# Kernel tuning notes

Measured on AMD Instinct MI355X. Metric: run time of the kernel, lower is better.

## Reference

```python
import jax, jax.numpy as jnp
import numpy as np

S, B, C = 7, 2, 20
LAMBDA_COORD = 5.0
LAMBDA_NOOBJ = 0.5
EPS = 1e-6


def _to_abs_xyxy(boxes):
    # boxes: [..., S, S, 4] cell-relative (x,y,w,h) -> normalized image (x1,y1,x2,y2)
    col = jnp.arange(S, dtype=boxes.dtype)            # broadcasts over last grid axis
    row = jnp.arange(S, dtype=boxes.dtype)[:, None]   # broadcasts over second-to-last grid axis
    x, y, w, h = boxes[..., 0], boxes[..., 1], boxes[..., 2], boxes[..., 3]
    cx = (col + x) / S
    cy = (row + y) / S
    return jnp.stack([cx - w / 2, cy - h / 2, cx + w / 2, cy + h / 2], axis=-1)


def _iou(a, b):
    # elementwise IoU of corresponding xyxy boxes (broadcasting allowed)
    x1 = jnp.maximum(a[..., 0], b[..., 0])
    y1 = jnp.maximum(a[..., 1], b[..., 1])
    x2 = jnp.minimum(a[..., 2], b[..., 2])
    y2 = jnp.minimum(a[..., 3], b[..., 3])
    inter = jnp.clip(x2 - x1, 0.0) * jnp.clip(y2 - y1, 0.0)
    area_a = (a[..., 2] - a[..., 0]) * (a[..., 3] - a[..., 1])
    area_b = (b[..., 2] - b[..., 0]) * (b[..., 3] - b[..., 1])
    return inter / (area_a + area_b - inter + EPS)


def setup_inputs() -> dict:
    key = jax.random.key(0)
    kp, kb, kf, kc = jax.random.split(key, 4)
    bs = 16384
    predictions = jax.random.uniform(kp, (bs, S, S, B * 5 + C), dtype=jnp.float32)
    gt_box = jax.random.uniform(kb, (bs, S, S, 4), dtype=jnp.float32)
    obj = (jax.random.uniform(kf, (bs, S, S)) < 0.06).astype(jnp.float32)
    cls = jax.nn.one_hot(jax.random.randint(kc, (bs, S, S), 0, C), C, dtype=jnp.float32)
    targets = jnp.concatenate([gt_box, obj[..., None], cls], axis=-1)
    return {"predictions": predictions, "targets": targets}


def reference(predictions, targets):
    bs = predictions.shape[0]
    pb = predictions[..., : B * 5].reshape(bs, S, S, B, 5)
    boxes = pb[..., :4]                 # [bs,S,S,B,4]
    confs = pb[..., 4]                  # [bs,S,S,B]
    logits = predictions[..., B * 5 :]  # [bs,S,S,C]

    gt_boxes = targets[..., :4]
    objf = (targets[..., 4] > 0).astype(predictions.dtype)  # [bs,S,S]
    gt_cls = targets[..., 5:]

    # IoU per candidate box vs the cell's GT box
    gt_abs = _to_abs_xyxy(gt_boxes)                         # [bs,S,S,4]
    pred_abs = _to_abs_xyxy(jnp.moveaxis(boxes, 3, 1))      # [bs,B,S,S,4]
    ious = jnp.moveaxis(_iou(pred_abs, gt_abs[:, None]), 1, 3)  # [bs,S,S,B]

    best = jnp.argmax(ious, axis=-1)                        # [bs,S,S]
    resp_box = jnp.take_along_axis(boxes, best[..., None, None], axis=3)[..., 0, :]  # [bs,S,S,4]
    resp_conf = jnp.take_along_axis(confs, best[..., None], axis=-1)[..., 0]
    resp_iou = jnp.take_along_axis(ious, best[..., None], axis=-1)[..., 0]

    # Localization loss (masked-sum == torch boolean-mask + sum reduction)
    w = objf[..., None]
    xy_loss = jnp.sum(w * (resp_box[..., :2] - gt_boxes[..., :2]) ** 2)
    wh_loss = jnp.sum(w * (jnp.sqrt(resp_box[..., 2:4] + EPS) - jnp.sqrt(gt_boxes[..., 2:4] + EPS)) ** 2)
    loss_coord = xy_loss + wh_loss

    # Objectness confidence: target is (detached) IoU of responsible box
    loss_conf_obj = jnp.sum(objf * (resp_conf - jax.lax.stop_gradient(resp_iou)) ** 2)

    # No-object confidence: every (cell, box) that is not the responsible box of an object cell
    resp_mask = jax.nn.one_hot(best, B, dtype=predictions.dtype) * objf[..., None]  # [bs,S,S,B]
    loss_conf_noobj = jnp.sum((1.0 - resp_mask) * confs ** 2)

    # Classification: cross-entropy with one-hot GT, summed over object cells
    logp = jax.nn.log_softmax(logits, axis=-1)
    loss_class = -jnp.sum(objf * jnp.sum(gt_cls * logp, axis=-1))

    n = jnp.asarray(bs, predictions.dtype)
    loss_total = (LAMBDA_COORD * loss_coord + loss_conf_obj + LAMBDA_NOOBJ * loss_conf_noobj + loss_class) / n
    # [loss_coord, loss_conf_obj, loss_conf_noobj, loss_class, loss_total]
    return jnp.stack([loss_coord / n, loss_conf_obj / n, loss_conf_noobj / n, loss_class / n, loss_total])
```

## Files before the change

kernel.cpp:

```cpp
#include <hip/hip_runtime.h>
#include <math.h>

namespace {
constexpr int S = 7;
constexpr int PF = 30;
constexpr int TF = 25;
constexpr int C = 20;
constexpr float EPS = 1e-6f;
constexpr float LAMBDA_COORD = 5.0f;
constexpr float LAMBDA_NOOBJ = 0.5f;
constexpr int BLK = 256;
constexpr int CPT = 4;
}

__global__ __launch_bounds__(BLK) void k_main(const float* __restrict__ pred,
                                              const float* __restrict__ tgt,
                                              float* __restrict__ part,
                                              int n_cells) {
    const int tid = threadIdx.x;
    const int base = blockIdx.x * (BLK * CPT) + tid;

    float2 a45[CPT], a89[CPT];
    float t4[CPT];
    bool ok[CPT];
    #pragma unroll
    for (int k = 0; k < CPT; ++k) {
        const int cell = base + k * BLK;
        ok[k] = (cell < n_cells);
        const float* p = pred + (size_t)cell * PF;
        const float* t = tgt + (size_t)cell * TF;
        if (ok[k]) {
            a45[k] = *(const float2*)(p + 4);
            a89[k] = *(const float2*)(p + 8);
            t4[k]  = t[4];
        } else {
            a45[k] = make_float2(0.f, 0.f);
            a89[k] = make_float2(0.f, 0.f);
            t4[k]  = 0.f;
        }
    }

    float v0 = 0.f, v1 = 0.f, v2 = 0.f, v3 = 0.f;
    #pragma unroll
    for (int k = 0; k < CPT; ++k) {
        const float c0 = a45[k].x, c1 = a89[k].y;
        v2 += c0 * c0 + c1 * c1;

        if (t4[k] > 0.f) {
            const int cell = base + k * BLK;
            const float* p = pred + (size_t)cell * PF;
            const float* t = tgt + (size_t)cell * TF;
            const int j = cell % S;
            const int i = (cell / S) % S;
            const float invS = 1.0f / (float)S;

            const float2 p01 = *(const float2*)(p + 0);
            const float2 p23 = *(const float2*)(p + 2);
            const float2 p67 = *(const float2*)(p + 6);
            const float gx = t[0], gy = t[1], gw = t[2], gh = t[3];

            const float gcx = ((float)j + gx) * invS;
            const float gcy = ((float)i + gy) * invS;
            const float gx1 = gcx - gw * 0.5f, gy1 = gcy - gh * 0.5f;
            const float gx2 = gcx + gw * 0.5f, gy2 = gcy + gh * 0.5f;
            const float garea = (gx2 - gx1) * (gy2 - gy1);

            const float bx[2]  = {p01.x, a45[k].y};
            const float by[2]  = {p01.y, p67.x};
            const float bw_[2] = {p23.x, p67.y};
            const float bh[2]  = {p23.y, a89[k].x};
            const float cf[2]  = {c0, c1};
            float iou[2];
            #pragma unroll
            for (int b = 0; b < 2; ++b) {
                const float cx = ((float)j + bx[b]) * invS;
                const float cy = ((float)i + by[b]) * invS;
                const float x1 = cx - bw_[b] * 0.5f, y1 = cy - bh[b] * 0.5f;
                const float x2 = cx + bw_[b] * 0.5f, y2 = cy + bh[b] * 0.5f;
                const float ix1 = fmaxf(x1, gx1), iy1 = fmaxf(y1, gy1);
                const float ix2 = fminf(x2, gx2), iy2 = fminf(y2, gy2);
                const float inter = fmaxf(ix2 - ix1, 0.f) * fmaxf(iy2 - iy1, 0.f);
                const float parea = (x2 - x1) * (y2 - y1);
                iou[b] = inter / (parea + garea - inter + EPS);
            }
            const int best = (iou[1] > iou[0]) ? 1 : 0;
            const float rconf = cf[best], riou = iou[best];

            const float dx = bx[best] - gx, dy = by[best] - gy;
            const float swd = sqrtf(bw_[best] + EPS) - sqrtf(gw + EPS);
            const float shd = sqrtf(bh[best] + EPS) - sqrtf(gh + EPS);
            v0 += dx * dx + dy * dy + swd * swd + shd * shd;
            const float dc = rconf - riou;
            v1 += dc * dc;
            v2 -= rconf * rconf;

            float se = 0.f, dot = 0.f, sg = 0.f;
            #pragma unroll
            for (int c = 0; c < C; c += 2) {
                const float2 lc = *(const float2*)(p + 10 + c);
                const float g0 = t[5 + c], g1 = t[6 + c];
                se  += __expf(lc.x) + __expf(lc.y);
                dot += g0 * lc.x + g1 * lc.y;
                sg  += g0 + g1;
            }
            v3 += __logf(se) * sg - dot;
        }
    }

    float v[4] = {v0, v1, v2, v3};
    #pragma unroll
    for (int off = 32; off >= 1; off >>= 1) {
        v[0] += __shfl_down(v[0], off, 64);
        v[1] += __shfl_down(v[1], off, 64);
        v[2] += __shfl_down(v[2], off, 64);
        v[3] += __shfl_down(v[3], off, 64);
    }
    __shared__ float red[16];
    if ((tid & 63) == 0) {
        const int wv = tid >> 6;
        red[wv * 4 + 0] = v[0];
        red[wv * 4 + 1] = v[1];
        red[wv * 4 + 2] = v[2];
        red[wv * 4 + 3] = v[3];
    }
    __syncthreads();
    if (tid < 4)
        part[blockIdx.x * 4 + tid] =
            red[tid] + red[4 + tid] + red[8 + tid] + red[12 + tid];
}

__global__ __launch_bounds__(BLK) void k_fin(const float* __restrict__ part,
                                             float* __restrict__ out,
                                             int nblk, float n) {
    const int tid = threadIdx.x;
    float a0 = 0.f, a1 = 0.f, a2 = 0.f, a3 = 0.f;
    for (int r = tid; r < nblk; r += BLK) {
        const float4 q = *(const float4*)(part + r * 4);
        a0 += q.x; a1 += q.y; a2 += q.z; a3 += q.w;
    }
    float v[4] = {a0, a1, a2, a3};
    #pragma unroll
    for (int off = 32; off >= 1; off >>= 1) {
        v[0] += __shfl_down(v[0], off, 64);
        v[1] += __shfl_down(v[1], off, 64);
        v[2] += __shfl_down(v[2], off, 64);
        v[3] += __shfl_down(v[3], off, 64);
    }
    __shared__ float red[16];
    if ((tid & 63) == 0) {
        const int wv = tid >> 6;
        red[wv * 4 + 0] = v[0];
        red[wv * 4 + 1] = v[1];
        red[wv * 4 + 2] = v[2];
        red[wv * 4 + 3] = v[3];
    }
    __syncthreads();
    if (tid == 0) {
        const float coord  = red[0] + red[4] + red[8] + red[12];
        const float cobj   = red[1] + red[5] + red[9] + red[13];
        const float cnoobj = red[2] + red[6] + red[10] + red[14];
        const float ccls   = red[3] + red[7] + red[11] + red[15];
        const float inv = 1.0f / n;
        out[0] = coord * inv;
        out[1] = cobj * inv;
        out[2] = cnoobj * inv;
        out[3] = ccls * inv;
        out[4] = (LAMBDA_COORD * coord + cobj + LAMBDA_NOOBJ * cnoobj + ccls) * inv;
    }
}

extern "C" void kernel_launch(void* const* d_in, const int* in_sizes, int n_in,
                              void* d_out, int out_size, void* d_ws, size_t ws_size,
                              hipStream_t stream) {
    const float* pred = (const float*)d_in[0];
    const float* tgt  = (const float*)d_in[1];
    float* out  = (float*)d_out;
    float* part = (float*)d_ws;

    const int n_cells = in_sizes[0] / PF;
    const float bs = (float)(n_cells / (S * S));
    const int nblk = (n_cells + BLK * CPT - 1) / (BLK * CPT);

    k_main<<<nblk, BLK, 0, stream>>>(pred, tgt, part, n_cells);
    k_fin<<<1, BLK, 0, stream>>>(part, out, nblk, bs);
}
```

Measured before the change: 213.5 us.

## Stage prediction tile through LDS with coalesced float4 loads, one cell per thread

Each block now copies its whole contiguous prediction tile (256 cells x 30 floats) into shared memory with coalesced float4 loads, then each thread reads its cell's fields from LDS. This replaces the earlier scheme of strided float2 loads with four cells per thread. The goal is to turn scattered, latency-bound global accesses into streaming ones. The cost is about 30KB of LDS per block, which limits occupancy, plus an extra barrier, and it loads the full prediction row even for no-object cells.

```diff
diff --git a/kernel.cpp b/kernel.cpp
--- a/kernel.cpp
+++ b/kernel.cpp
@@ -10,65 +10,54 @@
 constexpr float LAMBDA_COORD = 5.0f;
 constexpr float LAMBDA_NOOBJ = 0.5f;
 constexpr int BLK = 256;
-constexpr int CPT = 4;
+constexpr int TILE_F4 = BLK * PF / 4;
 }
 
-__global__ __launch_bounds__(BLK) void k_main(const float* __restrict__ pred,
+__global__ __launch_bounds__(BLK) void k_main(const float4* __restrict__ pred4,
                                               const float* __restrict__ tgt,
                                               float* __restrict__ part,
                                               int n_cells) {
+    __shared__ float sp[BLK * PF];
     const int tid = threadIdx.x;
-    const int base = blockIdx.x * (BLK * CPT) + tid;
+    const int cell = blockIdx.x * BLK + tid;
+    const bool ok = cell < n_cells;
 
-    float2 a45[CPT], a89[CPT];
-    float t4[CPT];
-    bool ok[CPT];
-    #pragma unroll
-    for (int k = 0; k < CPT; ++k) {
-        const int cell = base + k * BLK;
-        ok[k] = (cell < n_cells);
-        const float* p = pred + (size_t)cell * PF;
-        const float* t = tgt + (size_t)cell * TF;
-        if (ok[k]) {
-            a45[k] = *(const float2*)(p + 4);
-            a89[k] = *(const float2*)(p + 8);
-            t4[k]  = t[4];
-        } else {
-            a45[k] = make_float2(0.f, 0.f);
-            a89[k] = make_float2(0.f, 0.f);
-            t4[k]  = 0.f;
+    const float t4 = ok ? tgt[(size_t)cell * TF + 4] : 0.f;
+
+    {
+        const size_t base4 = (size_t)blockIdx.x * TILE_F4;
+        float4* s4 = (float4*)sp;
+        #pragma unroll
+        for (int k = 0; k < 8; ++k) {
+            const int idx = tid + k * BLK;
+            if (idx < TILE_F4) s4[idx] = pred4[base4 + idx];
         }
     }
+    __syncthreads();
 
     float v0 = 0.f, v1 = 0.f, v2 = 0.f, v3 = 0.f;
-    #pragma unroll
-    for (int k = 0; k < CPT; ++k) {
-        const float c0 = a45[k].x, c1 = a89[k].y;
-        v2 += c0 * c0 + c1 * c1;
+    if (ok) {
+        const float* p = sp + tid * PF;
+        const float c0 = p[4], c1 = p[9];
+        v2 = c0 * c0 + c1 * c1;
 
-        if (t4[k] > 0.f) {
-            const int cell = base + k * BLK;
-            const float* p = pred + (size_t)cell * PF;
+        if (t4 > 0.f) {
             const float* t = tgt + (size_t)cell * TF;
             const int j = cell % S;
             const int i = (cell / S) % S;
             const float invS = 1.0f / (float)S;
 
-            const float2 p01 = *(const float2*)(p + 0);
-            const float2 p23 = *(const float2*)(p + 2);
-            const float2 p67 = *(const float2*)(p + 6);
             const float gx = t[0], gy = t[1], gw = t[2], gh = t[3];
-
             const float gcx = ((float)j + gx) * invS;
             const float gcy = ((float)i + gy) * invS;
             const float gx1 = gcx - gw * 0.5f, gy1 = gcy - gh * 0.5f;
             const float gx2 = gcx + gw * 0.5f, gy2 = gcy + gh * 0.5f;
             const float garea = (gx2 - gx1) * (gy2 - gy1);
 
-            const float bx[2]  = {p01.x, a45[k].y};
-            const float by[2]  = {p01.y, p67.x};
-            const float bw_[2] = {p23.x, p67.y};
-            const float bh[2]  = {p23.y, a89[k].x};
+            const float bx[2]  = {p[0], p[5]};
+            const float by[2]  = {p[1], p[6]};
+            const float bw_[2] = {p[2], p[7]};
+            const float bh[2]  = {p[3], p[8]};
             const float cf[2]  = {c0, c1};
             float iou[2];
             #pragma unroll
@@ -89,21 +78,21 @@
             const float dx = bx[best] - gx, dy = by[best] - gy;
             const float swd = sqrtf(bw_[best] + EPS) - sqrtf(gw + EPS);
             const float shd = sqrtf(bh[best] + EPS) - sqrtf(gh + EPS);
-            v0 += dx * dx + dy * dy + swd * swd + shd * shd;
+            v0 = dx * dx + dy * dy + swd * swd + shd * shd;
             const float dc = rconf - riou;
-            v1 += dc * dc;
+            v1 = dc * dc;
             v2 -= rconf * rconf;
 
             float se = 0.f, dot = 0.f, sg = 0.f;
             #pragma unroll
             for (int c = 0; c < C; c += 2) {
-                const float2 lc = *(const float2*)(p + 10 + c);
-                const float g0 = t[5 + c], g1 = t[6 + c];
-                se  += __expf(lc.x) + __expf(lc.y);
-                dot += g0 * lc.x + g1 * lc.y;
+                const float l0 = p[10 + c], l1 = p[11 + c];
+                const float g0 = t[5 + c],  g1 = t[6 + c];
+                se  += __expf(l0) + __expf(l1);
+                dot += g0 * l0 + g1 * l1;
                 sg  += g0 + g1;
             }
-            v3 += __logf(se) * sg - dot;
+            v3 = __logf(se) * sg - dot;
         }
     }
 
@@ -115,18 +104,18 @@
         v[2] += __shfl_down(v[2], off, 64);
         v[3] += __shfl_down(v[3], off, 64);
     }
-    __shared__ float red[16];
+    __syncthreads();
     if ((tid & 63) == 0) {
         const int wv = tid >> 6;
-        red[wv * 4 + 0] = v[0];
-        red[wv * 4 + 1] = v[1];
-        red[wv * 4 + 2] = v[2];
-        red[wv * 4 + 3] = v[3];
+        sp[wv * 4 + 0] = v[0];
+        sp[wv * 4 + 1] = v[1];
+        sp[wv * 4 + 2] = v[2];
+        sp[wv * 4 + 3] = v[3];
     }
     __syncthreads();
     if (tid < 4)
         part[blockIdx.x * 4 + tid] =
-            red[tid] + red[4 + tid] + red[8 + tid] + red[12 + tid];
+            sp[tid] + sp[4 + tid] + sp[8 + tid] + sp[12 + tid];
 }
 
 __global__ __launch_bounds__(BLK) void k_fin(const float* __restrict__ part,
@@ -179,8 +168,8 @@
 
     const int n_cells = in_sizes[0] / PF;
     const float bs = (float)(n_cells / (S * S));
-    const int nblk = (n_cells + BLK * CPT - 1) / (BLK * CPT);
+    const int nblk = (n_cells + BLK - 1) / BLK;
 
-    k_main<<<nblk, BLK, 0, stream>>>(pred, tgt, part, n_cells);
+    k_main<<<nblk, BLK, 0, stream>>>((const float4*)pred, tgt, part, n_cells);
     k_fin<<<1, BLK, 0, stream>>>(part, out, nblk, bs);
 }
```

New measurement: 205.6 us. 3.7% less time.
